# Kernel tuning notes

Hardware: AMD Instinct MI355X
Metric: run time of the kernel (lower is better)

## Reference

```python
import jax, jax.numpy as jnp
import numpy as np

HEADS = 8
EPS = 1e-6


def _conv1x1(w, t):
    # w: [out_c, in_c], t: [B, in_c, L] -> [B, out_c, L]
    return jnp.einsum('oc,bcl->bol', w, t)


def setup_inputs() -> dict:
    key = jax.random.key(0)
    ks = jax.random.split(key, 9)
    B, C, H, W = 8, 256, 128, 128
    dim = C
    s = 1.0 / np.sqrt(dim)
    x = jax.random.normal(ks[0], (B, C, H, W), dtype=jnp.float32)
    y = jax.random.normal(ks[1], (B, 1, H // 2, W // 2), dtype=jnp.float32)
    wq_x = jax.random.normal(ks[2], (dim, dim), dtype=jnp.float32) * s
    wk_x = jax.random.normal(ks[3], (dim, dim), dtype=jnp.float32) * s
    wv = jax.random.normal(ks[4], (dim, dim), dtype=jnp.float32) * s
    wq_y = jax.random.normal(ks[5], (dim, 1), dtype=jnp.float32)
    wk_y = jax.random.normal(ks[6], (dim, 1), dtype=jnp.float32)
    w_out = jax.random.normal(ks[7], (dim, dim), dtype=jnp.float32) * s
    b_out = jnp.zeros((dim,), dtype=jnp.float32)
    return {"x": x, "y": y, "wq_x": wq_x, "wk_x": wk_x, "wv": wv,
            "wq_y": wq_y, "wk_y": wk_y, "w_out": w_out, "b_out": b_out}


def reference(x, y, wq_x, wk_x, wv, wq_y, wk_y, w_out, b_out):
    B, C, H, W = x.shape
    h = HEADS
    d = C // h
    L = H * W
    xr = x.reshape(B, C, L)

    # bilinear upsample y to (H, W); jax.image 'bilinear' == torch align_corners=False
    y_up = jax.image.resize(y, (B, 1, H, W), method='bilinear')
    yr = y_up.reshape(B, 1, L)

    q_x = _conv1x1(wq_x, xr).reshape(B, h, d, L)
    k_x = _conv1x1(wk_x, xr).reshape(B, h, d, L)
    v = _conv1x1(wv, xr).reshape(B, h, d, L)
    q_y = _conv1x1(wq_y, yr).reshape(B, h, d, L)
    k_y = _conv1x1(wk_y, yr).reshape(B, h, d, L)

    q = jax.nn.elu(q_x * q_y) + 1.0
    k = jax.nn.elu(k_x * k_y) + 1.0

    kv = jnp.einsum('bhcl,bhdl->bhcd', k, v)      # [B,h,d,d]
    k_sum = k.sum(axis=-1)                        # [B,h,d]
    z = 1.0 / (jnp.einsum('bhcl,bhc->bhl', q, k_sum) + EPS)  # [B,h,L]
    # faithful to torch: out[b,h,c,l] = q[b,h,c,l] * sum_d kv[b,h,c,d] * z[b,h,l]
    out = jnp.einsum('bhcl,bhcd,bhl->bhcl', q, kv, z)

    out = out.reshape(B, C, L)
    out = _conv1x1(w_out, out) + b_out[None, :, None]
    return out.reshape(B, C, H, W)
```

## Files before the change

### kernel.cpp

```cpp
#include <hip/hip_runtime.h>

typedef unsigned short u16;
typedef unsigned int   u32;
using short8   = __attribute__((ext_vector_type(8))) short;
using f32x4    = __attribute__((ext_vector_type(4))) float;
using ushort4v = __attribute__((ext_vector_type(4))) unsigned short;

#define CDIM 256
#define LDIM 16384
#define LT   128
#define NT   128
#define NB   8

__device__ __forceinline__ u16 f2bf(float f) {
  u32 u = __float_as_uint(f);
  u = (u + 0x7FFFu + ((u >> 16) & 1u)) >> 16;
  return (u16)u;
}

__global__ void k_prep(const float* __restrict__ wq_x, const float* __restrict__ wk_x,
                       const float* __restrict__ w_out, const float* __restrict__ wv,
                       const float* __restrict__ y,
                       u16* __restrict__ wqx_bf, u16* __restrict__ wkx_bf,
                       u16* __restrict__ wout_bf, u16* __restrict__ wvsum_bf,
                       float* __restrict__ yup) {
  int id = blockIdx.x * 256 + threadIdx.x;
  if (id < 65536) {
    wqx_bf[id]  = f2bf(wq_x[id]);
    wkx_bf[id]  = f2bf(wk_x[id]);
    wout_bf[id] = f2bf(w_out[id]);
  }
  if (id < 4096) {
    int r = id >> 8, c = id & 255;
    float s = 0.f;
    if (r < 8) {
      for (int d2 = 0; d2 < 32; ++d2) s += wv[(r * 32 + d2) * 256 + c];
    }
    wvsum_bf[id] = f2bf(s);
  }
  if (id < 131072) {
    int b = id >> 14, rem = id & 16383, i = rem >> 7, j = rem & 127;
    float si = 0.5f * i - 0.25f, sj = 0.5f * j - 0.25f;
    int i0 = (int)floorf(si), j0 = (int)floorf(sj);
    float fi = si - (float)i0, fj = sj - (float)j0;
    int i0c = i0 < 0 ? 0 : i0, i1c = i0 + 1 > 63 ? 63 : i0 + 1;
    int j0c = j0 < 0 ? 0 : j0, j1c = j0 + 1 > 63 ? 63 : j0 + 1;
    const float* yb = y + b * 4096;
    float v = (1.f - fi) * ((1.f - fj) * yb[i0c * 64 + j0c] + fj * yb[i0c * 64 + j1c])
            +        fi  * ((1.f - fj) * yb[i1c * 64 + j0c] + fj * yb[i1c * 64 + j1c]);
    yup[id] = v;
  }
}

__device__ __forceinline__ void stage_x(u32* x_lds, const float* __restrict__ x,
                                        int b, int l0, int tid) {
  int cp = tid & 127, half = tid >> 7;
  const float4* r0 = (const float4*)(x + ((size_t)(b * 256 + 2 * cp)) * LDIM + l0 + half * 64);
  const float4* r1 = (const float4*)((const float*)r0 + LDIM);
#pragma unroll 4
  for (int j4 = 0; j4 < 16; ++j4) {
    float4 v0 = r0[j4], v1 = r1[j4];
    int lb = half * 64 + j4 * 4;
    x_lds[(lb + 0) * 132 + cp] = (u32)f2bf(v0.x) | ((u32)f2bf(v1.x) << 16);
    x_lds[(lb + 1) * 132 + cp] = (u32)f2bf(v0.y) | ((u32)f2bf(v1.y) << 16);
    x_lds[(lb + 2) * 132 + cp] = (u32)f2bf(v0.z) | ((u32)f2bf(v1.z) << 16);
    x_lds[(lb + 3) * 132 + cp] = (u32)f2bf(v0.w) | ((u32)f2bf(v1.w) << 16);
  }
}

__global__ __launch_bounds__(256, 2) void k_pass1(
    const float* __restrict__ x, const u16* __restrict__ wkx_bf,
    const u16* __restrict__ wvsum_bf, const float* __restrict__ wk_y,
    const float* __restrict__ yup, float* __restrict__ part) {
  __shared__ u32 x_lds[128 * 132];
  __shared__ float vsum_lds[8 * 128];
  __shared__ float yup_lds[128];
  __shared__ float wky_lds[256];

  int tid = threadIdx.x, bid = blockIdx.x;
  int b = bid >> 7, tile = bid & 127;
  int l0 = tile * LT;

  if (tid < 128) yup_lds[tid] = yup[b * LDIM + l0 + tid];
  wky_lds[tid] = wk_y[tid];
  stage_x(x_lds, x, b, l0, tid);
  __syncthreads();

  int lane = tid & 63, wave = tid >> 6;
  int lid = lane & 15, g = lane >> 4;
  int wb = wave * 64;
  const u16* xl = (const u16*)x_lds;

  f32x4 z4 = {0.f, 0.f, 0.f, 0.f};
  f32x4 acc[4][8];
#pragma unroll
  for (int i = 0; i < 4; ++i)
#pragma unroll
    for (int j = 0; j < 8; ++j) acc[i][j] = z4;
  f32x4 vacc[2] = {z4, z4};

  for (int kk = 0; kk < 8; ++kk) {
    int kof = kk * 32 + g * 8;
    short8 a[4];
#pragma unroll
    for (int fm = 0; fm < 4; ++fm)
      a[fm] = *(const short8*)(wkx_bf + (size_t)(wb + fm * 16 + lid) * 256 + kof);
    short8 av = *(const short8*)(wvsum_bf + (size_t)lid * 256 + kof);
#pragma unroll
    for (int fn = 0; fn < 8; ++fn) {
      short8 bb = *(const short8*)(xl + (fn * 16 + lid) * 264 + kof);
#pragma unroll
      for (int fm = 0; fm < 4; ++fm)
        acc[fm][fn] = __builtin_amdgcn_mfma_f32_16x16x32_bf16(a[fm], bb, acc[fm][fn], 0, 0, 0);
    }
#pragma unroll
    for (int fv = 0; fv < 2; ++fv) {
      int fn = wave * 2 + fv;
      short8 bb = *(const short8*)(xl + (fn * 16 + lid) * 264 + kof);
      vacc[fv] = __builtin_amdgcn_mfma_f32_16x16x32_bf16(av, bb, vacc[fv], 0, 0, 0);
    }
  }
  if (g < 2) {
#pragma unroll
    for (int fv = 0; fv < 2; ++fv)
#pragma unroll
      for (int r = 0; r < 4; ++r)
        vsum_lds[(g * 4 + r) * 128 + (wave * 2 + fv) * 16 + lid] = vacc[fv][r];
  }
  __syncthreads();

  float wky_r[4][4];
#pragma unroll
  for (int fm = 0; fm < 4; ++fm)
#pragma unroll
    for (int r = 0; r < 4; ++r) wky_r[fm][r] = wky_lds[wb + fm * 16 + g * 4 + r];

  float s1[4][4], s2[4][4];
#pragma unroll
  for (int fm = 0; fm < 4; ++fm)
#pragma unroll
    for (int r = 0; r < 4; ++r) { s1[fm][r] = 0.f; s2[fm][r] = 0.f; }

#pragma unroll
  for (int fn = 0; fn < 8; ++fn) {
    float yv = yup_lds[fn * 16 + lid];
#pragma unroll
    for (int fm = 0; fm < 4; ++fm) {
      float vs = vsum_lds[(wave * 2 + (fm >> 1)) * 128 + fn * 16 + lid];
#pragma unroll
      for (int r = 0; r < 4; ++r) {
        float v = acc[fm][fn][r] * (wky_r[fm][r] * yv);
        float k = v > 0.f ? v + 1.f : __expf(v);
        s1[fm][r] += k;
        s2[fm][r] += k * vs;
      }
    }
  }
#pragma unroll
  for (int fm = 0; fm < 4; ++fm)
#pragma unroll
    for (int r = 0; r < 4; ++r) {
      float a1 = s1[fm][r], a2 = s2[fm][r];
#pragma unroll
      for (int off = 1; off < 16; off <<= 1) {
        a1 += __shfl_xor(a1, off);
        a2 += __shfl_xor(a2, off);
      }
      if (lid == 0) {
        int c = wb + fm * 16 + g * 4 + r;
        part[(size_t)bid * 512 + c]       = a1;
        part[(size_t)bid * 512 + 256 + c] = a2;
      }
    }
}

__global__ void k_reduce(const float* __restrict__ part,
                         float* __restrict__ ksum, float* __restrict__ kvs) {
  int b = blockIdx.x, c = threadIdx.x;
  float s1 = 0.f, s2 = 0.f;
  for (int t = 0; t < NT; ++t) {
    s1 += part[(size_t)(b * NT + t) * 512 + c];
    s2 += part[(size_t)(b * NT + t) * 512 + 256 + c];
  }
  ksum[b * 256 + c] = s1;
  kvs[b * 256 + c] = s2;
}

__global__ __launch_bounds__(256, 2) void k_pass2(
    const float* __restrict__ x, const u16* __restrict__ wqx_bf,
    const u16* __restrict__ wout_bf, const float* __restrict__ wq_y,
    const float* __restrict__ yup, const float* __restrict__ ksum,
    const float* __restrict__ kvs, const float* __restrict__ b_out,
    float* __restrict__ out) {
  __shared__ u32 x_lds[128 * 132];
  __shared__ float yup_lds[128];
  __shared__ float wqy_lds[256];
  __shared__ float ksum_lds[256];
  __shared__ float kvs_lds[256];
  __shared__ float bout_lds[256];

  int tid = threadIdx.x, bid = blockIdx.x;
  int b = bid >> 7, tile = bid & 127;
  int l0 = tile * LT;

  if (tid < 128) yup_lds[tid] = yup[b * LDIM + l0 + tid];
  wqy_lds[tid]  = wq_y[tid];
  ksum_lds[tid] = ksum[b * 256 + tid];
  kvs_lds[tid]  = kvs[b * 256 + tid];
  bout_lds[tid] = b_out[tid];
  stage_x(x_lds, x, b, l0, tid);
  __syncthreads();

  int lane = tid & 63, wave = tid >> 6;
  int lid = lane & 15, g = lane >> 4;
  int wb = wave * 64;
  u16* xl = (u16*)x_lds;

  f32x4 z4 = {0.f, 0.f, 0.f, 0.f};
  f32x4 acc[4][8];
#pragma unroll
  for (int i = 0; i < 4; ++i)
#pragma unroll
    for (int j = 0; j < 8; ++j) acc[i][j] = z4;

  for (int kk = 0; kk < 8; ++kk) {
    int kof = kk * 32 + g * 8;
    short8 a[4];
#pragma unroll
    for (int fm = 0; fm < 4; ++fm)
      a[fm] = *(const short8*)(wqx_bf + (size_t)(wb + fm * 16 + lid) * 256 + kof);
#pragma unroll
    for (int fn = 0; fn < 8; ++fn) {
      short8 bb = *(const short8*)((const u16*)xl + (fn * 16 + lid) * 264 + kof);
#pragma unroll
      for (int fm = 0; fm < 4; ++fm)
        acc[fm][fn] = __builtin_amdgcn_mfma_f32_16x16x32_bf16(a[fm], bb, acc[fm][fn], 0, 0, 0);
    }
  }
  __syncthreads();

  float wqy_r[4][4], ks_r[4][4], kv_r[4][4];
#pragma unroll
  for (int fm = 0; fm < 4; ++fm)
#pragma unroll
    for (int r = 0; r < 4; ++r) {
      int c = wb + fm * 16 + g * 4 + r;
      wqy_r[fm][r] = wqy_lds[c];
      ks_r[fm][r]  = ksum_lds[c];
      kv_r[fm][r]  = kvs_lds[c];
    }

#pragma unroll
  for (int fn = 0; fn < 8; ++fn) {
    float yv = yup_lds[fn * 16 + lid];
    float q[4][4];
    float d0 = 0.f, d1 = 0.f;
#pragma unroll
    for (int fm = 0; fm < 4; ++fm)
#pragma unroll
      for (int r = 0; r < 4; ++r) {
        float v = acc[fm][fn][r] * (wqy_r[fm][r] * yv);
        float qq = v > 0.f ? v + 1.f : __expf(v);
        q[fm][r] = qq;
        if (fm < 2) d0 += qq * ks_r[fm][r]; else d1 += qq * ks_r[fm][r];
      }
    d0 += __shfl_xor(d0, 16); d0 += __shfl_xor(d0, 32);
    d1 += __shfl_xor(d1, 16); d1 += __shfl_xor(d1, 32);
    float zz0 = 1.f / (d0 + 1e-6f), zz1 = 1.f / (d1 + 1e-6f);
    int l = fn * 16 + lid;
#pragma unroll
    for (int fm = 0; fm < 4; ++fm) {
      float zz = fm < 2 ? zz0 : zz1;
      ushort4v tw;
#pragma unroll
      for (int r = 0; r < 4; ++r) tw[r] = f2bf(q[fm][r] * kv_r[fm][r] * zz);
      *(ushort4v*)((u16*)xl + l * 264 + wb + fm * 16 + g * 4) = tw;
    }
  }
  __syncthreads();

#pragma unroll
  for (int i = 0; i < 4; ++i)
#pragma unroll
    for (int j = 0; j < 8; ++j) acc[i][j] = z4;
  for (int kk = 0; kk < 8; ++kk) {
    int kof = kk * 32 + g * 8;
    short8 a[4];
#pragma unroll
    for (int fm = 0; fm < 4; ++fm)
      a[fm] = *(const short8*)(wout_bf + (size_t)(wb + fm * 16 + lid) * 256 + kof);
#pragma unroll
    for (int fn = 0; fn < 8; ++fn) {
      short8 bb = *(const short8*)((const u16*)xl + (fn * 16 + lid) * 264 + kof);
#pragma unroll
      for (int fm = 0; fm < 4; ++fm)
        acc[fm][fn] = __builtin_amdgcn_mfma_f32_16x16x32_bf16(a[fm], bb, acc[fm][fn], 0, 0, 0);
    }
  }

#pragma unroll
  for (int fm = 0; fm < 4; ++fm) {
#pragma unroll
    for (int r = 0; r < 4; ++r) {
      int o = wb + fm * 16 + g * 4 + r;
      float bo = bout_lds[o];
      size_t base = ((size_t)b * 256 + o) * LDIM + l0;
#pragma unroll
      for (int fn = 0; fn < 8; ++fn)
        out[base + fn * 16 + lid] = acc[fm][fn][r] + bo;
    }
  }
}

extern "C" void kernel_launch(void* const* d_in, const int* in_sizes, int n_in,
                              void* d_out, int out_size, void* d_ws, size_t ws_size,
                              hipStream_t stream) {
  const float* x     = (const float*)d_in[0];
  const float* y     = (const float*)d_in[1];
  const float* wq_x  = (const float*)d_in[2];
  const float* wk_x  = (const float*)d_in[3];
  const float* wv    = (const float*)d_in[4];
  const float* wq_y  = (const float*)d_in[5];
  const float* wk_y  = (const float*)d_in[6];
  const float* w_out = (const float*)d_in[7];
  const float* b_out = (const float*)d_in[8];
  float* out = (float*)d_out;

  char* ws = (char*)d_ws;
  float* yup      = (float*)(ws + 0);
  u16*   wqx_bf   = (u16*)(ws + 524288);
  u16*   wkx_bf   = (u16*)(ws + 655360);
  u16*   wout_bf  = (u16*)(ws + 786432);
  u16*   wvsum_bf = (u16*)(ws + 917504);
  float* ksum     = (float*)(ws + 925696);
  float* kvs      = (float*)(ws + 933888);
  float* part     = (float*)(ws + 942080);

  k_prep<<<512, 256, 0, stream>>>(wq_x, wk_x, w_out, wv, y,
                                  wqx_bf, wkx_bf, wout_bf, wvsum_bf, yup);
  k_pass1<<<NB * NT, 256, 0, stream>>>(x, wkx_bf, wvsum_bf, wk_y, yup, part);
  k_reduce<<<NB, 256, 0, stream>>>(part, ksum, kvs);
  k_pass2<<<NB * NT, 256, 0, stream>>>(x, wqx_bf, wout_bf, wq_y, yup,
                                       ksum, kvs, b_out, out);
}
```

Before: 146.7 us.

## Cache bf16 swizzled x tile in workspace for pass2 via direct global-to-LDS loads

Pass1 now writes its bf16-converted, XOR-swizzled x tile to a workspace buffer when the workspace is large enough. Pass2 then loads that buffer straight into LDS with global_load_lds instead of re-reading fp32 x and converting it again. This roughly halves pass2's x read traffic and drops its conversion work, but adds a bf16 write of x in pass1. The LDS layout also changes from padded rows to an XOR swizzle, and conversion moves to packed bf16x2 intrinsics. All of this depends on ws_size being large enough, otherwise pass2 falls back to restaging from fp32 x.

```diff
diff --git a/kernel.cpp b/kernel.cpp
--- a/kernel.cpp
+++ b/kernel.cpp
@@ -1,10 +1,12 @@
 #include <hip/hip_runtime.h>
+#include <hip/hip_bf16.h>
 
 typedef unsigned short u16;
 typedef unsigned int   u32;
 using short8   = __attribute__((ext_vector_type(8))) short;
 using f32x4    = __attribute__((ext_vector_type(4))) float;
 using ushort4v = __attribute__((ext_vector_type(4))) unsigned short;
+using u32x2    = __attribute__((ext_vector_type(2))) unsigned int;
 
 #define CDIM 256
 #define LDIM 16384
@@ -16,6 +18,11 @@
   u32 u = __float_as_uint(f);
   u = (u + 0x7FFFu + ((u >> 16) & 1u)) >> 16;
   return (u16)u;
+}
+
+__device__ __forceinline__ u32 pk2(float a, float b) {
+  __hip_bfloat162 h = __float22bfloat162_rn(make_float2(a, b));
+  return *(u32*)&h;
 }
 
 __global__ void k_prep(const float* __restrict__ wq_x, const float* __restrict__ wk_x,
@@ -52,30 +59,52 @@
   }
 }
 
-__device__ __forceinline__ void stage_x(u32* x_lds, const float* __restrict__ x,
-                                        int b, int l0, int tid) {
-  int cp = tid & 127, half = tid >> 7;
-  const float4* r0 = (const float4*)(x + ((size_t)(b * 256 + 2 * cp)) * LDIM + l0 + half * 64);
-  const float4* r1 = (const float4*)((const float*)r0 + LDIM);
-#pragma unroll 4
-  for (int j4 = 0; j4 < 16; ++j4) {
-    float4 v0 = r0[j4], v1 = r1[j4];
-    int lb = half * 64 + j4 * 4;
-    x_lds[(lb + 0) * 132 + cp] = (u32)f2bf(v0.x) | ((u32)f2bf(v1.x) << 16);
-    x_lds[(lb + 1) * 132 + cp] = (u32)f2bf(v0.y) | ((u32)f2bf(v1.y) << 16);
-    x_lds[(lb + 2) * 132 + cp] = (u32)f2bf(v0.z) | ((u32)f2bf(v1.z) << 16);
-    x_lds[(lb + 3) * 132 + cp] = (u32)f2bf(v0.w) | ((u32)f2bf(v1.w) << 16);
-  }
+template<bool DUMP>
+__device__ __forceinline__ void stage_f32(char* xl, const float* __restrict__ x,
+                                          u16* __restrict__ xt,
+                                          int b, int l0, int tid) {
+  int cp = tid & 63, lg = tid >> 6;
+  const float* xr = x + ((size_t)b * 256 + 4 * cp) * LDIM + l0 + lg * 32;
+  char* xtp = (char*)xt + ((size_t)b * LDIM + l0) * 512;
+  int sl = cp >> 1, sub = (cp & 1) * 8;
+#pragma unroll
+  for (int j4 = 0; j4 < 8; ++j4) {
+    float4 v0 = *(const float4*)(xr + 0 * LDIM + j4 * 4);
+    float4 v1 = *(const float4*)(xr + 1 * LDIM + j4 * 4);
+    float4 v2 = *(const float4*)(xr + 2 * LDIM + j4 * 4);
+    float4 v3 = *(const float4*)(xr + 3 * LDIM + j4 * 4);
+    const float* f0 = (const float*)&v0;
+    const float* f1 = (const float*)&v1;
+    const float* f2 = (const float*)&v2;
+    const float* f3 = (const float*)&v3;
+#pragma unroll
+    for (int e = 0; e < 4; ++e) {
+      int ll = lg * 32 + j4 * 4 + e;
+      u32x2 val;
+      val.x = pk2(f0[e], f1[e]);
+      val.y = pk2(f2[e], f3[e]);
+      size_t off = (size_t)ll * 512 + (size_t)((sl ^ (ll & 7)) * 16 + sub);
+      *(u32x2*)(xl + off) = val;
+      if (DUMP) *(u32x2*)(xtp + off) = val;
+    }
+  }
+}
+
+__device__ __forceinline__ short8 frag_b(const char* xl, int ll, int kk, int g) {
+  int slot = (kk * 4 + g) ^ (ll & 7);
+  return *(const short8*)(xl + (size_t)ll * 512 + slot * 16);
 }
 
 __global__ __launch_bounds__(256, 2) void k_pass1(
     const float* __restrict__ x, const u16* __restrict__ wkx_bf,
     const u16* __restrict__ wvsum_bf, const float* __restrict__ wk_y,
-    const float* __restrict__ yup, float* __restrict__ part) {
-  __shared__ u32 x_lds[128 * 132];
+    const float* __restrict__ yup, u16* __restrict__ xt,
+    float* __restrict__ part, int dump) {
+  __shared__ f32x4 x_lds4[4096];
   __shared__ float vsum_lds[8 * 128];
   __shared__ float yup_lds[128];
   __shared__ float wky_lds[256];
+  char* xl = (char*)x_lds4;
 
   int tid = threadIdx.x, bid = blockIdx.x;
   int b = bid >> 7, tile = bid & 127;
@@ -83,13 +112,13 @@
 
   if (tid < 128) yup_lds[tid] = yup[b * LDIM + l0 + tid];
   wky_lds[tid] = wk_y[tid];
-  stage_x(x_lds, x, b, l0, tid);
+  if (dump) stage_f32<true>(xl, x, xt, b, l0, tid);
+  else      stage_f32<false>(xl, x, xt, b, l0, tid);
   __syncthreads();
 
   int lane = tid & 63, wave = tid >> 6;
   int lid = lane & 15, g = lane >> 4;
   int wb = wave * 64;
-  const u16* xl = (const u16*)x_lds;
 
   f32x4 z4 = {0.f, 0.f, 0.f, 0.f};
   f32x4 acc[4][8];
@@ -108,15 +137,14 @@
     short8 av = *(const short8*)(wvsum_bf + (size_t)lid * 256 + kof);
 #pragma unroll
     for (int fn = 0; fn < 8; ++fn) {
-      short8 bb = *(const short8*)(xl + (fn * 16 + lid) * 264 + kof);
+      short8 bb = frag_b(xl, fn * 16 + lid, kk, g);
 #pragma unroll
       for (int fm = 0; fm < 4; ++fm)
         acc[fm][fn] = __builtin_amdgcn_mfma_f32_16x16x32_bf16(a[fm], bb, acc[fm][fn], 0, 0, 0);
     }
 #pragma unroll
     for (int fv = 0; fv < 2; ++fv) {
-      int fn = wave * 2 + fv;
-      short8 bb = *(const short8*)(xl + (fn * 16 + lid) * 264 + kof);
+      short8 bb = frag_b(xl, (wave * 2 + fv) * 16 + lid, kk, g);
       vacc[fv] = __builtin_amdgcn_mfma_f32_16x16x32_bf16(av, bb, vacc[fv], 0, 0, 0);
     }
   }
@@ -187,34 +215,47 @@
 }
 
 __global__ __launch_bounds__(256, 2) void k_pass2(
-    const float* __restrict__ x, const u16* __restrict__ wqx_bf,
-    const u16* __restrict__ wout_bf, const float* __restrict__ wq_y,
-    const float* __restrict__ yup, const float* __restrict__ ksum,
-    const float* __restrict__ kvs, const float* __restrict__ b_out,
-    float* __restrict__ out) {
-  __shared__ u32 x_lds[128 * 132];
+    const float* __restrict__ x, const u16* __restrict__ xt,
+    const u16* __restrict__ wqx_bf, const u16* __restrict__ wout_bf,
+    const float* __restrict__ wq_y, const float* __restrict__ yup,
+    const float* __restrict__ ksum, const float* __restrict__ kvs,
+    const float* __restrict__ b_out, float* __restrict__ out, int use_xt) {
+  __shared__ f32x4 x_lds4[4096];
   __shared__ float yup_lds[128];
   __shared__ float wqy_lds[256];
   __shared__ float ksum_lds[256];
   __shared__ float kvs_lds[256];
   __shared__ float bout_lds[256];
+  char* xl = (char*)x_lds4;
 
   int tid = threadIdx.x, bid = blockIdx.x;
   int b = bid >> 7, tile = bid & 127;
   int l0 = tile * LT;
+  int lane = tid & 63, wave = tid >> 6;
 
   if (tid < 128) yup_lds[tid] = yup[b * LDIM + l0 + tid];
   wqy_lds[tid]  = wq_y[tid];
   ksum_lds[tid] = ksum[b * 256 + tid];
   kvs_lds[tid]  = kvs[b * 256 + tid];
   bout_lds[tid] = b_out[tid];
-  stage_x(x_lds, x, b, l0, tid);
-  __syncthreads();
-
-  int lane = tid & 63, wave = tid >> 6;
+
+  if (use_xt) {
+    const char* gsrc = (const char*)xt + ((size_t)b * LDIM + l0) * 512;
+#pragma unroll
+    for (int it = 0; it < 16; ++it) {
+      int cidx = it * 4 + wave;
+      __builtin_amdgcn_global_load_lds(
+          (const __attribute__((address_space(1))) void*)(gsrc + cidx * 1024 + lane * 16),
+          (__attribute__((address_space(3))) void*)(xl + cidx * 1024),
+          16, 0, 0);
+    }
+  } else {
+    stage_f32<false>(xl, x, (u16*)nullptr, b, l0, tid);
+  }
+  __syncthreads();
+
   int lid = lane & 15, g = lane >> 4;
   int wb = wave * 64;
-  u16* xl = (u16*)x_lds;
 
   f32x4 z4 = {0.f, 0.f, 0.f, 0.f};
   f32x4 acc[4][8];
@@ -231,7 +272,7 @@
       a[fm] = *(const short8*)(wqx_bf + (size_t)(wb + fm * 16 + lid) * 256 + kof);
 #pragma unroll
     for (int fn = 0; fn < 8; ++fn) {
-      short8 bb = *(const short8*)((const u16*)xl + (fn * 16 + lid) * 264 + kof);
+      short8 bb = frag_b(xl, fn * 16 + lid, kk, g);
 #pragma unroll
       for (int fm = 0; fm < 4; ++fm)
         acc[fm][fn] = __builtin_amdgcn_mfma_f32_16x16x32_bf16(a[fm], bb, acc[fm][fn], 0, 0, 0);
@@ -267,14 +308,15 @@
     d0 += __shfl_xor(d0, 16); d0 += __shfl_xor(d0, 32);
     d1 += __shfl_xor(d1, 16); d1 += __shfl_xor(d1, 32);
     float zz0 = 1.f / (d0 + 1e-6f), zz1 = 1.f / (d1 + 1e-6f);
-    int l = fn * 16 + lid;
+    int ll = fn * 16 + lid;
 #pragma unroll
     for (int fm = 0; fm < 4; ++fm) {
       float zz = fm < 2 ? zz0 : zz1;
       ushort4v tw;
 #pragma unroll
       for (int r = 0; r < 4; ++r) tw[r] = f2bf(q[fm][r] * kv_r[fm][r] * zz);
-      *(ushort4v*)((u16*)xl + l * 264 + wb + fm * 16 + g * 4) = tw;
+      int slot = (wave * 8 + fm * 2 + (g >> 1)) ^ (ll & 7);
+      *(ushort4v*)(xl + (size_t)ll * 512 + slot * 16 + (g & 1) * 8) = tw;
     }
   }
   __syncthreads();
@@ -291,7 +333,7 @@
       a[fm] = *(const short8*)(wout_bf + (size_t)(wb + fm * 16 + lid) * 256 + kof);
 #pragma unroll
     for (int fn = 0; fn < 8; ++fn) {
-      short8 bb = *(const short8*)((const u16*)xl + (fn * 16 + lid) * 264 + kof);
+      short8 bb = frag_b(xl, fn * 16 + lid, kk, g);
 #pragma unroll
       for (int fm = 0; fm < 4; ++fm)
         acc[fm][fn] = __builtin_amdgcn_mfma_f32_16x16x32_bf16(a[fm], bb, acc[fm][fn], 0, 0, 0);
@@ -335,11 +377,15 @@
   float* ksum     = (float*)(ws + 925696);
   float* kvs      = (float*)(ws + 933888);
   float* part     = (float*)(ws + 942080);
+  u16*   xt       = (u16*)(ws + 4194304);
+
+  const size_t ws_need = 4194304 + (size_t)NB * LDIM * 512;
+  int use_xt = ws_size >= ws_need ? 1 : 0;
 
   k_prep<<<512, 256, 0, stream>>>(wq_x, wk_x, w_out, wv, y,
                                   wqx_bf, wkx_bf, wout_bf, wvsum_bf, yup);
-  k_pass1<<<NB * NT, 256, 0, stream>>>(x, wkx_bf, wvsum_bf, wk_y, yup, part);
+  k_pass1<<<NB * NT, 256, 0, stream>>>(x, wkx_bf, wvsum_bf, wk_y, yup, xt, part, use_xt);
   k_reduce<<<NB, 256, 0, stream>>>(part, ksum, kvs);
-  k_pass2<<<NB * NT, 256, 0, stream>>>(x, wqx_bf, wout_bf, wq_y, yup,
-                                       ksum, kvs, b_out, out);
-}
+  k_pass2<<<NB * NT, 256, 0, stream>>>(x, xt, wqx_bf, wout_bf, wq_y, yup,
+                                       ksum, kvs, b_out, out, use_xt);
+}
```

After: 166.5 us. 1.13x slower.

## Swizzle LDS x tile, double waves per block, parallelize reduce

Applied to the files above, without the earlier changes.

Replaces the padded LDS layout for the bf16 x tile with an XOR-swizzled 16-byte-slot layout. Staging now writes 16-byte vectors using packed bf16 conversion, and fragment reads use the same swizzle, which aims to cut bank conflicts and narrow LDS stores. Blocks grow to 512 threads (8 waves, each owning 32 output channels), which halves accumulator registers per wave to raise occupancy and latency hiding. k_reduce uses 1024 threads with a two-way split so each batch's partial reduction runs on more threads. The trade-off is more waves contending for the same LDS tile and more redundant weight-fragment loads per block.

```diff
diff --git a/kernel.cpp b/kernel.cpp
--- a/kernel.cpp
+++ b/kernel.cpp
@@ -1,10 +1,11 @@
 #include <hip/hip_runtime.h>
+#include <hip/hip_bf16.h>
 
 typedef unsigned short u16;
 typedef unsigned int   u32;
 using short8   = __attribute__((ext_vector_type(8))) short;
 using f32x4    = __attribute__((ext_vector_type(4))) float;
-using ushort4v = __attribute__((ext_vector_type(4))) unsigned short;
+using u32x4    = __attribute__((ext_vector_type(4))) unsigned int;
 
 #define CDIM 256
 #define LDIM 16384
@@ -16,6 +17,20 @@
   u32 u = __float_as_uint(f);
   u = (u + 0x7FFFu + ((u >> 16) & 1u)) >> 16;
   return (u16)u;
+}
+
+__device__ __forceinline__ u32 pk2(float a, float b) {
+  __hip_bfloat162 h = __float22bfloat162_rn(make_float2(a, b));
+  return *(u32*)&h;
+}
+
+__device__ __forceinline__ int swz(int l) {
+  return ((l >> 2) & 31) ^ ((l & 3) << 2);
+}
+
+__device__ __forceinline__ short8 frag_b(const char* xl, int ll, int kk, int g) {
+  int slot = (kk * 4 + g) ^ swz(ll);
+  return *(const short8*)(xl + (size_t)ll * 512 + slot * 16);
 }
 
 __global__ void k_prep(const float* __restrict__ wq_x, const float* __restrict__ wk_x,
@@ -52,112 +67,121 @@
   }
 }
 
-__device__ __forceinline__ void stage_x(u32* x_lds, const float* __restrict__ x,
+__device__ __forceinline__ void stage_x(char* xl, const float* __restrict__ x,
                                         int b, int l0, int tid) {
-  int cp = tid & 127, half = tid >> 7;
-  const float4* r0 = (const float4*)(x + ((size_t)(b * 256 + 2 * cp)) * LDIM + l0 + half * 64);
-  const float4* r1 = (const float4*)((const float*)r0 + LDIM);
-#pragma unroll 4
-  for (int j4 = 0; j4 < 16; ++j4) {
-    float4 v0 = r0[j4], v1 = r1[j4];
-    int lb = half * 64 + j4 * 4;
-    x_lds[(lb + 0) * 132 + cp] = (u32)f2bf(v0.x) | ((u32)f2bf(v1.x) << 16);
-    x_lds[(lb + 1) * 132 + cp] = (u32)f2bf(v0.y) | ((u32)f2bf(v1.y) << 16);
-    x_lds[(lb + 2) * 132 + cp] = (u32)f2bf(v0.z) | ((u32)f2bf(v1.z) << 16);
-    x_lds[(lb + 3) * 132 + cp] = (u32)f2bf(v0.w) | ((u32)f2bf(v1.w) << 16);
-  }
-}
-
-__global__ __launch_bounds__(256, 2) void k_pass1(
+  int k = tid & 31, cg = tid >> 5;
+  const float* bp = x + ((size_t)b * 256 + cg * 8) * LDIM + l0 + k * 4;
+#pragma unroll
+  for (int it = 0; it < 2; ++it) {
+    const float* p = bp + (size_t)(128 * it) * LDIM;
+    float4 r0 = *(const float4*)(p + 0 * LDIM);
+    float4 r1 = *(const float4*)(p + 1 * LDIM);
+    float4 r2 = *(const float4*)(p + 2 * LDIM);
+    float4 r3 = *(const float4*)(p + 3 * LDIM);
+    float4 r4 = *(const float4*)(p + 4 * LDIM);
+    float4 r5 = *(const float4*)(p + 5 * LDIM);
+    float4 r6 = *(const float4*)(p + 6 * LDIM);
+    float4 r7 = *(const float4*)(p + 7 * LDIM);
+    int sl = cg + 16 * it;
+    const float* f0 = (const float*)&r0; const float* f1 = (const float*)&r1;
+    const float* f2 = (const float*)&r2; const float* f3 = (const float*)&r3;
+    const float* f4 = (const float*)&r4; const float* f5 = (const float*)&r5;
+    const float* f6 = (const float*)&r6; const float* f7 = (const float*)&r7;
+#pragma unroll
+    for (int e = 0; e < 4; ++e) {
+      int l = k * 4 + e;
+      u32x4 wv;
+      wv.x = pk2(f0[e], f1[e]);
+      wv.y = pk2(f2[e], f3[e]);
+      wv.z = pk2(f4[e], f5[e]);
+      wv.w = pk2(f6[e], f7[e]);
+      int slot = sl ^ swz(l);
+      *(u32x4*)(xl + (size_t)l * 512 + slot * 16) = wv;
+    }
+  }
+}
+
+__global__ __launch_bounds__(512, 4) void k_pass1(
     const float* __restrict__ x, const u16* __restrict__ wkx_bf,
     const u16* __restrict__ wvsum_bf, const float* __restrict__ wk_y,
     const float* __restrict__ yup, float* __restrict__ part) {
-  __shared__ u32 x_lds[128 * 132];
+  __shared__ u32x4 xbuf[4096];
   __shared__ float vsum_lds[8 * 128];
   __shared__ float yup_lds[128];
   __shared__ float wky_lds[256];
+  char* xl = (char*)xbuf;
 
   int tid = threadIdx.x, bid = blockIdx.x;
   int b = bid >> 7, tile = bid & 127;
   int l0 = tile * LT;
 
   if (tid < 128) yup_lds[tid] = yup[b * LDIM + l0 + tid];
-  wky_lds[tid] = wk_y[tid];
-  stage_x(x_lds, x, b, l0, tid);
-  __syncthreads();
-
-  int lane = tid & 63, wave = tid >> 6;
+  if (tid < 256) wky_lds[tid] = wk_y[tid];
+  stage_x(xl, x, b, l0, tid);
+  __syncthreads();
+
+  int lane = tid & 63, w = tid >> 6;
   int lid = lane & 15, g = lane >> 4;
-  int wb = wave * 64;
-  const u16* xl = (const u16*)x_lds;
+  int wb = w * 32;
 
   f32x4 z4 = {0.f, 0.f, 0.f, 0.f};
-  f32x4 acc[4][8];
-#pragma unroll
-  for (int i = 0; i < 4; ++i)
+  f32x4 acc[2][8];
+#pragma unroll
+  for (int i = 0; i < 2; ++i)
 #pragma unroll
     for (int j = 0; j < 8; ++j) acc[i][j] = z4;
-  f32x4 vacc[2] = {z4, z4};
+  f32x4 vacc = z4;
 
   for (int kk = 0; kk < 8; ++kk) {
     int kof = kk * 32 + g * 8;
-    short8 a[4];
-#pragma unroll
-    for (int fm = 0; fm < 4; ++fm)
-      a[fm] = *(const short8*)(wkx_bf + (size_t)(wb + fm * 16 + lid) * 256 + kof);
+    short8 a0 = *(const short8*)(wkx_bf + (size_t)(wb + lid) * 256 + kof);
+    short8 a1 = *(const short8*)(wkx_bf + (size_t)(wb + 16 + lid) * 256 + kof);
     short8 av = *(const short8*)(wvsum_bf + (size_t)lid * 256 + kof);
 #pragma unroll
     for (int fn = 0; fn < 8; ++fn) {
-      short8 bb = *(const short8*)(xl + (fn * 16 + lid) * 264 + kof);
-#pragma unroll
-      for (int fm = 0; fm < 4; ++fm)
-        acc[fm][fn] = __builtin_amdgcn_mfma_f32_16x16x32_bf16(a[fm], bb, acc[fm][fn], 0, 0, 0);
-    }
-#pragma unroll
-    for (int fv = 0; fv < 2; ++fv) {
-      int fn = wave * 2 + fv;
-      short8 bb = *(const short8*)(xl + (fn * 16 + lid) * 264 + kof);
-      vacc[fv] = __builtin_amdgcn_mfma_f32_16x16x32_bf16(av, bb, vacc[fv], 0, 0, 0);
-    }
+      short8 bb = frag_b(xl, fn * 16 + lid, kk, g);
+      acc[0][fn] = __builtin_amdgcn_mfma_f32_16x16x32_bf16(a0, bb, acc[0][fn], 0, 0, 0);
+      acc[1][fn] = __builtin_amdgcn_mfma_f32_16x16x32_bf16(a1, bb, acc[1][fn], 0, 0, 0);
+    }
+    short8 bv = frag_b(xl, w * 16 + lid, kk, g);
+    vacc = __builtin_amdgcn_mfma_f32_16x16x32_bf16(av, bv, vacc, 0, 0, 0);
   }
   if (g < 2) {
 #pragma unroll
-    for (int fv = 0; fv < 2; ++fv)
-#pragma unroll
-      for (int r = 0; r < 4; ++r)
-        vsum_lds[(g * 4 + r) * 128 + (wave * 2 + fv) * 16 + lid] = vacc[fv][r];
-  }
-  __syncthreads();
-
-  float wky_r[4][4];
-#pragma unroll
-  for (int fm = 0; fm < 4; ++fm)
+    for (int r = 0; r < 4; ++r)
+      vsum_lds[(g * 4 + r) * 128 + w * 16 + lid] = vacc[r];
+  }
+  __syncthreads();
+
+  float wky_r[2][4];
+#pragma unroll
+  for (int fm = 0; fm < 2; ++fm)
 #pragma unroll
     for (int r = 0; r < 4; ++r) wky_r[fm][r] = wky_lds[wb + fm * 16 + g * 4 + r];
 
-  float s1[4][4], s2[4][4];
-#pragma unroll
-  for (int fm = 0; fm < 4; ++fm)
+  float s1[2][4], s2[2][4];
+#pragma unroll
+  for (int fm = 0; fm < 2; ++fm)
 #pragma unroll
     for (int r = 0; r < 4; ++r) { s1[fm][r] = 0.f; s2[fm][r] = 0.f; }
 
 #pragma unroll
   for (int fn = 0; fn < 8; ++fn) {
-    float yv = yup_lds[fn * 16 + lid];
-#pragma unroll
-    for (int fm = 0; fm < 4; ++fm) {
-      float vs = vsum_lds[(wave * 2 + (fm >> 1)) * 128 + fn * 16 + lid];
+    int l = fn * 16 + lid;
+    float yv = yup_lds[l];
+    float vs = vsum_lds[w * 128 + l];
+#pragma unroll
+    for (int fm = 0; fm < 2; ++fm)
 #pragma unroll
       for (int r = 0; r < 4; ++r) {
         float v = acc[fm][fn][r] * (wky_r[fm][r] * yv);
-        float k = v > 0.f ? v + 1.f : __expf(v);
-        s1[fm][r] += k;
-        s2[fm][r] += k * vs;
+        float kq = v > 0.f ? v + 1.f : __expf(v);
+        s1[fm][r] += kq;
+        s2[fm][r] += kq * vs;
       }
-    }
-  }
-#pragma unroll
-  for (int fm = 0; fm < 4; ++fm)
+  }
+#pragma unroll
+  for (int fm = 0; fm < 2; ++fm)
 #pragma unroll
     for (int r = 0; r < 4; ++r) {
       float a1 = s1[fm][r], a2 = s2[fm][r];
@@ -174,74 +198,78 @@
     }
 }
 
-__global__ void k_reduce(const float* __restrict__ part,
-                         float* __restrict__ ksum, float* __restrict__ kvs) {
-  int b = blockIdx.x, c = threadIdx.x;
-  float s1 = 0.f, s2 = 0.f;
-  for (int t = 0; t < NT; ++t) {
-    s1 += part[(size_t)(b * NT + t) * 512 + c];
-    s2 += part[(size_t)(b * NT + t) * 512 + 256 + c];
-  }
-  ksum[b * 256 + c] = s1;
-  kvs[b * 256 + c] = s2;
-}
-
-__global__ __launch_bounds__(256, 2) void k_pass2(
+__global__ __launch_bounds__(1024) void k_reduce(
+    const float* __restrict__ part, float* __restrict__ ksum, float* __restrict__ kvs) {
+  __shared__ float red[2][512];
+  int b = blockIdx.x, tid = threadIdx.x;
+  int u = tid & 511, h = tid >> 9;
+  float s = 0.f;
+  for (int j = 0; j < 64; ++j)
+    s += part[(size_t)(b * NT + h * 64 + j) * 512 + u];
+  red[h][u] = s;
+  __syncthreads();
+  if (tid < 512) {
+    float t = red[0][tid] + red[1][tid];
+    if (tid < 256) ksum[b * 256 + tid] = t;
+    else           kvs[b * 256 + tid - 256] = t;
+  }
+}
+
+__global__ __launch_bounds__(512, 4) void k_pass2(
     const float* __restrict__ x, const u16* __restrict__ wqx_bf,
     const u16* __restrict__ wout_bf, const float* __restrict__ wq_y,
     const float* __restrict__ yup, const float* __restrict__ ksum,
     const float* __restrict__ kvs, const float* __restrict__ b_out,
     float* __restrict__ out) {
-  __shared__ u32 x_lds[128 * 132];
+  __shared__ u32x4 xbuf[4096];
   __shared__ float yup_lds[128];
   __shared__ float wqy_lds[256];
   __shared__ float ksum_lds[256];
   __shared__ float kvs_lds[256];
   __shared__ float bout_lds[256];
+  char* xl = (char*)xbuf;
 
   int tid = threadIdx.x, bid = blockIdx.x;
   int b = bid >> 7, tile = bid & 127;
   int l0 = tile * LT;
 
   if (tid < 128) yup_lds[tid] = yup[b * LDIM + l0 + tid];
-  wqy_lds[tid]  = wq_y[tid];
-  ksum_lds[tid] = ksum[b * 256 + tid];
-  kvs_lds[tid]  = kvs[b * 256 + tid];
-  bout_lds[tid] = b_out[tid];
-  stage_x(x_lds, x, b, l0, tid);
-  __syncthreads();
-
-  int lane = tid & 63, wave = tid >> 6;
+  if (tid < 256) {
+    wqy_lds[tid]  = wq_y[tid];
+    ksum_lds[tid] = ksum[b * 256 + tid];
+    kvs_lds[tid]  = kvs[b * 256 + tid];
+    bout_lds[tid] = b_out[tid];
+  }
+  stage_x(xl, x, b, l0, tid);
+  __syncthreads();
+
+  int lane = tid & 63, w = tid >> 6;
   int lid = lane & 15, g = lane >> 4;
-  int wb = wave * 64;
-  u16* xl = (u16*)x_lds;
+  int wb = w * 32;
 
   f32x4 z4 = {0.f, 0.f, 0.f, 0.f};
-  f32x4 acc[4][8];
-#pragma unroll
-  for (int i = 0; i < 4; ++i)
+  f32x4 acc[2][8];
+#pragma unroll
+  for (int i = 0; i < 2; ++i)
 #pragma unroll
     for (int j = 0; j < 8; ++j) acc[i][j] = z4;
 
   for (int kk = 0; kk < 8; ++kk) {
     int kof = kk * 32 + g * 8;
-    short8 a[4];
-#pragma unroll
-    for (int fm = 0; fm < 4; ++fm)
-      a[fm] = *(const short8*)(wqx_bf + (size_t)(wb + fm * 16 + lid) * 256 + kof);
+    short8 a0 = *(const short8*)(wqx_bf + (size_t)(wb + lid) * 256 + kof);
+    short8 a1 = *(const short8*)(wqx_bf + (size_t)(wb + 16 + lid) * 256 + kof);
 #pragma unroll
     for (int fn = 0; fn < 8; ++fn) {
-      short8 bb = *(const short8*)((const u16*)xl + (fn * 16 + lid) * 264 + kof);
-#pragma unroll
-      for (int fm = 0; fm < 4; ++fm)
-        acc[fm][fn] = __builtin_amdgcn_mfma_f32_16x16x32_bf16(a[fm], bb, acc[fm][fn], 0, 0, 0);
-    }
-  }
-  __syncthreads();
-
-  float wqy_r[4][4], ks_r[4][4], kv_r[4][4];
-#pragma unroll
-  for (int fm = 0; fm < 4; ++fm)
+      short8 bb = frag_b(xl, fn * 16 + lid, kk, g);
+      acc[0][fn] = __builtin_amdgcn_mfma_f32_16x16x32_bf16(a0, bb, acc[0][fn], 0, 0, 0);
+      acc[1][fn] = __builtin_amdgcn_mfma_f32_16x16x32_bf16(a1, bb, acc[1][fn], 0, 0, 0);
+    }
+  }
+  __syncthreads();
+
+  float wqy_r[2][4], ks_r[2][4], kv_r[2][4];
+#pragma unroll
+  for (int fm = 0; fm < 2; ++fm)
 #pragma unroll
     for (int r = 0; r < 4; ++r) {
       int c = wb + fm * 16 + g * 4 + r;
@@ -252,54 +280,52 @@
 
 #pragma unroll
   for (int fn = 0; fn < 8; ++fn) {
-    float yv = yup_lds[fn * 16 + lid];
-    float q[4][4];
-    float d0 = 0.f, d1 = 0.f;
-#pragma unroll
-    for (int fm = 0; fm < 4; ++fm)
+    int l = fn * 16 + lid;
+    float yv = yup_lds[l];
+    float q[2][4];
+    float d = 0.f;
+#pragma unroll
+    for (int fm = 0; fm < 2; ++fm)
 #pragma unroll
       for (int r = 0; r < 4; ++r) {
         float v = acc[fm][fn][r] * (wqy_r[fm][r] * yv);
         float qq = v > 0.f ? v + 1.f : __expf(v);
         q[fm][r] = qq;
-        if (fm < 2) d0 += qq * ks_r[fm][r]; else d1 += qq * ks_r[fm][r];
+        d += qq * ks_r[fm][r];
       }
-    d0 += __shfl_xor(d0, 16); d0 += __shfl_xor(d0, 32);
-    d1 += __shfl_xor(d1, 16); d1 += __shfl_xor(d1, 32);
-    float zz0 = 1.f / (d0 + 1e-6f), zz1 = 1.f / (d1 + 1e-6f);
-    int l = fn * 16 + lid;
-#pragma unroll
-    for (int fm = 0; fm < 4; ++fm) {
-      float zz = fm < 2 ? zz0 : zz1;
-      ushort4v tw;
-#pragma unroll
-      for (int r = 0; r < 4; ++r) tw[r] = f2bf(q[fm][r] * kv_r[fm][r] * zz);
-      *(ushort4v*)((u16*)xl + l * 264 + wb + fm * 16 + g * 4) = tw;
-    }
-  }
-  __syncthreads();
-
-#pragma unroll
-  for (int i = 0; i < 4; ++i)
+    d += __shfl_xor(d, 16); d += __shfl_xor(d, 32);
+    float zz = 1.f / (d + 1e-6f);
+    int sl = w * 4 + (g >> 1);
+#pragma unroll
+    for (int fm = 0; fm < 2; ++fm) {
+      u32 w0 = pk2(q[fm][0] * kv_r[fm][0] * zz, q[fm][1] * kv_r[fm][1] * zz);
+      u32 w1 = pk2(q[fm][2] * kv_r[fm][2] * zz, q[fm][3] * kv_r[fm][3] * zz);
+      int slot = (sl + fm * 2) ^ swz(l);
+      char* p = xl + (size_t)l * 512 + slot * 16 + (g & 1) * 8;
+      *(u32*)p = w0;
+      *(u32*)(p + 4) = w1;
+    }
+  }
+  __syncthreads();
+
+#pragma unroll
+  for (int i = 0; i < 2; ++i)
 #pragma unroll
     for (int j = 0; j < 8; ++j) acc[i][j] = z4;
   for (int kk = 0; kk < 8; ++kk) {
     int kof = kk * 32 + g * 8;
-    short8 a[4];
-#pragma unroll
-    for (int fm = 0; fm < 4; ++fm)
-      a[fm] = *(const short8*)(wout_bf + (size_t)(wb + fm * 16 + lid) * 256 + kof);
+    short8 a0 = *(const short8*)(wout_bf + (size_t)(wb + lid) * 256 + kof);
+    short8 a1 = *(const short8*)(wout_bf + (size_t)(wb + 16 + lid) * 256 + kof);
 #pragma unroll
     for (int fn = 0; fn < 8; ++fn) {
-      short8 bb = *(const short8*)((const u16*)xl + (fn * 16 + lid) * 264 + kof);
-#pragma unroll
-      for (int fm = 0; fm < 4; ++fm)
-        acc[fm][fn] = __builtin_amdgcn_mfma_f32_16x16x32_bf16(a[fm], bb, acc[fm][fn], 0, 0, 0);
-    }
-  }
-
-#pragma unroll
-  for (int fm = 0; fm < 4; ++fm) {
+      short8 bb = frag_b(xl, fn * 16 + lid, kk, g);
+      acc[0][fn] = __builtin_amdgcn_mfma_f32_16x16x32_bf16(a0, bb, acc[0][fn], 0, 0, 0);
+      acc[1][fn] = __builtin_amdgcn_mfma_f32_16x16x32_bf16(a1, bb, acc[1][fn], 0, 0, 0);
+    }
+  }
+
+#pragma unroll
+  for (int fm = 0; fm < 2; ++fm) {
 #pragma unroll
     for (int r = 0; r < 4; ++r) {
       int o = wb + fm * 16 + g * 4 + r;
@@ -338,8 +364,8 @@
 
   k_prep<<<512, 256, 0, stream>>>(wq_x, wk_x, w_out, wv, y,
                                   wqx_bf, wkx_bf, wout_bf, wvsum_bf, yup);
-  k_pass1<<<NB * NT, 256, 0, stream>>>(x, wkx_bf, wvsum_bf, wk_y, yup, part);
-  k_reduce<<<NB, 256, 0, stream>>>(part, ksum, kvs);
-  k_pass2<<<NB * NT, 256, 0, stream>>>(x, wqx_bf, wout_bf, wq_y, yup,
+  k_pass1<<<NB * NT, 512, 0, stream>>>(x, wkx_bf, wvsum_bf, wk_y, yup, part);
+  k_reduce<<<NB, 1024, 0, stream>>>(part, ksum, kvs);
+  k_pass2<<<NB * NT, 512, 0, stream>>>(x, wqx_bf, wout_bf, wq_y, yup,
                                        ksum, kvs, b_out, out);
 }
```

New measurement: 263.7 us. 1.8x slower.

## Use XOR-swizzled unpadded LDS layout for x tile and widen reduce

Applied to the files above, without the earlier changes.

Replaces the padded 132-word-stride LDS tile with a 512-byte-row layout whose 16-byte slots are XOR-swizzled by position. Staging now loads 8 channels per thread and writes 16-byte packed bf16 vectors, so LDS stores are wider and bank conflicts are fewer. Fragment reads and the pass-2 intermediate writeback use the same swizzle. The reduce kernel now launches 1024 threads to split the tile sum into two halves, at the cost of extra shared-memory combining and a different global load pattern in staging.

```diff
diff --git a/kernel.cpp b/kernel.cpp
--- a/kernel.cpp
+++ b/kernel.cpp
@@ -1,10 +1,12 @@
 #include <hip/hip_runtime.h>
+#include <hip/hip_bf16.h>
 
 typedef unsigned short u16;
 typedef unsigned int   u32;
 using short8   = __attribute__((ext_vector_type(8))) short;
 using f32x4    = __attribute__((ext_vector_type(4))) float;
 using ushort4v = __attribute__((ext_vector_type(4))) unsigned short;
+using u32x4    = __attribute__((ext_vector_type(4))) unsigned int;
 
 #define CDIM 256
 #define LDIM 16384
@@ -16,6 +18,20 @@
   u32 u = __float_as_uint(f);
   u = (u + 0x7FFFu + ((u >> 16) & 1u)) >> 16;
   return (u16)u;
+}
+
+__device__ __forceinline__ u32 pk2(float a, float b) {
+  __hip_bfloat162 h = __float22bfloat162_rn(make_float2(a, b));
+  return *(u32*)&h;
+}
+
+__device__ __forceinline__ int swz(int l) {
+  return ((l >> 2) & 31) ^ ((l & 3) << 2);
+}
+
+__device__ __forceinline__ short8 frag_b(const char* xl, int ll, int kk, int g) {
+  int slot = (kk * 4 + g) ^ swz(ll);
+  return *(const short8*)(xl + (size_t)ll * 512 + slot * 16);
 }
 
 __global__ void k_prep(const float* __restrict__ wq_x, const float* __restrict__ wk_x,
@@ -52,19 +68,37 @@
   }
 }
 
-__device__ __forceinline__ void stage_x(u32* x_lds, const float* __restrict__ x,
+__device__ __forceinline__ void stage_x(char* xl, const float* __restrict__ x,
                                         int b, int l0, int tid) {
-  int cp = tid & 127, half = tid >> 7;
-  const float4* r0 = (const float4*)(x + ((size_t)(b * 256 + 2 * cp)) * LDIM + l0 + half * 64);
-  const float4* r1 = (const float4*)((const float*)r0 + LDIM);
-#pragma unroll 4
-  for (int j4 = 0; j4 < 16; ++j4) {
-    float4 v0 = r0[j4], v1 = r1[j4];
-    int lb = half * 64 + j4 * 4;
-    x_lds[(lb + 0) * 132 + cp] = (u32)f2bf(v0.x) | ((u32)f2bf(v1.x) << 16);
-    x_lds[(lb + 1) * 132 + cp] = (u32)f2bf(v0.y) | ((u32)f2bf(v1.y) << 16);
-    x_lds[(lb + 2) * 132 + cp] = (u32)f2bf(v0.z) | ((u32)f2bf(v1.z) << 16);
-    x_lds[(lb + 3) * 132 + cp] = (u32)f2bf(v0.w) | ((u32)f2bf(v1.w) << 16);
+  int k = tid & 31, co = tid >> 5;
+  const float* bp = x + ((size_t)b * 256 + co * 8) * LDIM + l0 + k * 4;
+#pragma unroll
+  for (int oi = 0; oi < 4; ++oi) {
+    const float* p = bp + (size_t)(oi * 64) * LDIM;
+    float4 r0 = *(const float4*)(p + 0 * LDIM);
+    float4 r1 = *(const float4*)(p + 1 * LDIM);
+    float4 r2 = *(const float4*)(p + 2 * LDIM);
+    float4 r3 = *(const float4*)(p + 3 * LDIM);
+    float4 r4 = *(const float4*)(p + 4 * LDIM);
+    float4 r5 = *(const float4*)(p + 5 * LDIM);
+    float4 r6 = *(const float4*)(p + 6 * LDIM);
+    float4 r7 = *(const float4*)(p + 7 * LDIM);
+    const float* f0 = (const float*)&r0; const float* f1 = (const float*)&r1;
+    const float* f2 = (const float*)&r2; const float* f3 = (const float*)&r3;
+    const float* f4 = (const float*)&r4; const float* f5 = (const float*)&r5;
+    const float* f6 = (const float*)&r6; const float* f7 = (const float*)&r7;
+    int so = co + oi * 8;
+#pragma unroll
+    for (int e = 0; e < 4; ++e) {
+      int l = k * 4 + e;
+      u32x4 wv;
+      wv.x = pk2(f0[e], f1[e]);
+      wv.y = pk2(f2[e], f3[e]);
+      wv.z = pk2(f4[e], f5[e]);
+      wv.w = pk2(f6[e], f7[e]);
+      int slot = so ^ swz(l);
+      *(u32x4*)(xl + (size_t)l * 512 + slot * 16) = wv;
+    }
   }
 }
 
@@ -72,10 +106,11 @@
     const float* __restrict__ x, const u16* __restrict__ wkx_bf,
     const u16* __restrict__ wvsum_bf, const float* __restrict__ wk_y,
     const float* __restrict__ yup, float* __restrict__ part) {
-  __shared__ u32 x_lds[128 * 132];
+  __shared__ u32x4 xbuf[4096];
   __shared__ float vsum_lds[8 * 128];
   __shared__ float yup_lds[128];
   __shared__ float wky_lds[256];
+  char* xl = (char*)xbuf;
 
   int tid = threadIdx.x, bid = blockIdx.x;
   int b = bid >> 7, tile = bid & 127;
@@ -83,13 +118,12 @@
 
   if (tid < 128) yup_lds[tid] = yup[b * LDIM + l0 + tid];
   wky_lds[tid] = wk_y[tid];
-  stage_x(x_lds, x, b, l0, tid);
+  stage_x(xl, x, b, l0, tid);
   __syncthreads();
 
   int lane = tid & 63, wave = tid >> 6;
   int lid = lane & 15, g = lane >> 4;
   int wb = wave * 64;
-  const u16* xl = (const u16*)x_lds;
 
   f32x4 z4 = {0.f, 0.f, 0.f, 0.f};
   f32x4 acc[4][8];
@@ -108,15 +142,14 @@
     short8 av = *(const short8*)(wvsum_bf + (size_t)lid * 256 + kof);
 #pragma unroll
     for (int fn = 0; fn < 8; ++fn) {
-      short8 bb = *(const short8*)(xl + (fn * 16 + lid) * 264 + kof);
+      short8 bb = frag_b(xl, fn * 16 + lid, kk, g);
 #pragma unroll
       for (int fm = 0; fm < 4; ++fm)
         acc[fm][fn] = __builtin_amdgcn_mfma_f32_16x16x32_bf16(a[fm], bb, acc[fm][fn], 0, 0, 0);
     }
 #pragma unroll
     for (int fv = 0; fv < 2; ++fv) {
-      int fn = wave * 2 + fv;
-      short8 bb = *(const short8*)(xl + (fn * 16 + lid) * 264 + kof);
+      short8 bb = frag_b(xl, (wave * 2 + fv) * 16 + lid, kk, g);
       vacc[fv] = __builtin_amdgcn_mfma_f32_16x16x32_bf16(av, bb, vacc[fv], 0, 0, 0);
     }
   }
@@ -143,16 +176,17 @@
 
 #pragma unroll
   for (int fn = 0; fn < 8; ++fn) {
-    float yv = yup_lds[fn * 16 + lid];
+    int l = fn * 16 + lid;
+    float yv = yup_lds[l];
 #pragma unroll
     for (int fm = 0; fm < 4; ++fm) {
-      float vs = vsum_lds[(wave * 2 + (fm >> 1)) * 128 + fn * 16 + lid];
+      float vs = vsum_lds[(wave * 2 + (fm >> 1)) * 128 + l];
 #pragma unroll
       for (int r = 0; r < 4; ++r) {
         float v = acc[fm][fn][r] * (wky_r[fm][r] * yv);
-        float k = v > 0.f ? v + 1.f : __expf(v);
-        s1[fm][r] += k;
-        s2[fm][r] += k * vs;
+        float kq = v > 0.f ? v + 1.f : __expf(v);
+        s1[fm][r] += kq;
+        s2[fm][r] += kq * vs;
       }
     }
   }
@@ -174,16 +208,21 @@
     }
 }
 
-__global__ void k_reduce(const float* __restrict__ part,
-                         float* __restrict__ ksum, float* __restrict__ kvs) {
-  int b = blockIdx.x, c = threadIdx.x;
-  float s1 = 0.f, s2 = 0.f;
-  for (int t = 0; t < NT; ++t) {
-    s1 += part[(size_t)(b * NT + t) * 512 + c];
-    s2 += part[(size_t)(b * NT + t) * 512 + 256 + c];
-  }
-  ksum[b * 256 + c] = s1;
-  kvs[b * 256 + c] = s2;
+__global__ __launch_bounds__(1024) void k_reduce(
+    const float* __restrict__ part, float* __restrict__ ksum, float* __restrict__ kvs) {
+  __shared__ float red[2][512];
+  int b = blockIdx.x, tid = threadIdx.x;
+  int u = tid & 511, h = tid >> 9;
+  float s = 0.f;
+  for (int j = 0; j < 64; ++j)
+    s += part[(size_t)(b * NT + h * 64 + j) * 512 + u];
+  red[h][u] = s;
+  __syncthreads();
+  if (tid < 512) {
+    float t = red[0][tid] + red[1][tid];
+    if (tid < 256) ksum[b * 256 + tid] = t;
+    else           kvs[b * 256 + tid - 256] = t;
+  }
 }
 
 __global__ __launch_bounds__(256, 2) void k_pass2(
@@ -192,12 +231,13 @@
     const float* __restrict__ yup, const float* __restrict__ ksum,
     const float* __restrict__ kvs, const float* __restrict__ b_out,
     float* __restrict__ out) {
-  __shared__ u32 x_lds[128 * 132];
+  __shared__ u32x4 xbuf[4096];
   __shared__ float yup_lds[128];
   __shared__ float wqy_lds[256];
   __shared__ float ksum_lds[256];
   __shared__ float kvs_lds[256];
   __shared__ float bout_lds[256];
+  char* xl = (char*)xbuf;
 
   int tid = threadIdx.x, bid = blockIdx.x;
   int b = bid >> 7, tile = bid & 127;
@@ -208,13 +248,12 @@
   ksum_lds[tid] = ksum[b * 256 + tid];
   kvs_lds[tid]  = kvs[b * 256 + tid];
   bout_lds[tid] = b_out[tid];
-  stage_x(x_lds, x, b, l0, tid);
+  stage_x(xl, x, b, l0, tid);
   __syncthreads();
 
   int lane = tid & 63, wave = tid >> 6;
   int lid = lane & 15, g = lane >> 4;
   int wb = wave * 64;
-  u16* xl = (u16*)x_lds;
 
   f32x4 z4 = {0.f, 0.f, 0.f, 0.f};
   f32x4 acc[4][8];
@@ -231,7 +270,7 @@
       a[fm] = *(const short8*)(wqx_bf + (size_t)(wb + fm * 16 + lid) * 256 + kof);
 #pragma unroll
     for (int fn = 0; fn < 8; ++fn) {
-      short8 bb = *(const short8*)((const u16*)xl + (fn * 16 + lid) * 264 + kof);
+      short8 bb = frag_b(xl, fn * 16 + lid, kk, g);
 #pragma unroll
       for (int fm = 0; fm < 4; ++fm)
         acc[fm][fn] = __builtin_amdgcn_mfma_f32_16x16x32_bf16(a[fm], bb, acc[fm][fn], 0, 0, 0);
@@ -252,7 +291,8 @@
 
 #pragma unroll
   for (int fn = 0; fn < 8; ++fn) {
-    float yv = yup_lds[fn * 16 + lid];
+    int l = fn * 16 + lid;
+    float yv = yup_lds[l];
     float q[4][4];
     float d0 = 0.f, d1 = 0.f;
 #pragma unroll
@@ -267,14 +307,14 @@
     d0 += __shfl_xor(d0, 16); d0 += __shfl_xor(d0, 32);
     d1 += __shfl_xor(d1, 16); d1 += __shfl_xor(d1, 32);
     float zz0 = 1.f / (d0 + 1e-6f), zz1 = 1.f / (d1 + 1e-6f);
-    int l = fn * 16 + lid;
 #pragma unroll
     for (int fm = 0; fm < 4; ++fm) {
       float zz = fm < 2 ? zz0 : zz1;
       ushort4v tw;
 #pragma unroll
       for (int r = 0; r < 4; ++r) tw[r] = f2bf(q[fm][r] * kv_r[fm][r] * zz);
-      *(ushort4v*)((u16*)xl + l * 264 + wb + fm * 16 + g * 4) = tw;
+      int slot = (wave * 8 + fm * 2 + (g >> 1)) ^ swz(l);
+      *(ushort4v*)(xl + (size_t)l * 512 + slot * 16 + (g & 1) * 8) = tw;
     }
   }
   __syncthreads();
@@ -291,7 +331,7 @@
       a[fm] = *(const short8*)(wout_bf + (size_t)(wb + fm * 16 + lid) * 256 + kof);
 #pragma unroll
     for (int fn = 0; fn < 8; ++fn) {
-      short8 bb = *(const short8*)((const u16*)xl + (fn * 16 + lid) * 264 + kof);
+      short8 bb = frag_b(xl, fn * 16 + lid, kk, g);
 #pragma unroll
       for (int fm = 0; fm < 4; ++fm)
         acc[fm][fn] = __builtin_amdgcn_mfma_f32_16x16x32_bf16(a[fm], bb, acc[fm][fn], 0, 0, 0);
@@ -339,7 +379,7 @@
   k_prep<<<512, 256, 0, stream>>>(wq_x, wk_x, w_out, wv, y,
                                   wqx_bf, wkx_bf, wout_bf, wvsum_bf, yup);
   k_pass1<<<NB * NT, 256, 0, stream>>>(x, wkx_bf, wvsum_bf, wk_y, yup, part);
-  k_reduce<<<NB, 256, 0, stream>>>(part, ksum, kvs);
+  k_reduce<<<NB, 1024, 0, stream>>>(part, ksum, kvs);
   k_pass2<<<NB * NT, 256, 0, stream>>>(x, wqx_bf, wout_bf, wq_y, yup,
                                        ksum, kvs, b_out, out);
 }
```

Measured after the change: 153.0 us. +4.3%, slower.
